# Optimization experiments

Hardware: AMD Instinct MI355X
Metric: run time of the kernel (lower is better)

Reference implementation:

```python
import jax, jax.numpy as jnp
import numpy as np

N = 100000
E = 1600000
IN_C, HID_C, OUT_C = 64, 128, 64


def sage_conv(x, edge_index, W_l, b_l, W_r):
    # PyG SAGEConv (mean aggr): out = lin_l(mean_{j in N(i)} x_j) + lin_r(x_i)
    src, dst = edge_index[0], edge_index[1]
    n = x.shape[0]
    msg = x[src]                                        # [E, C] gather
    agg = jax.ops.segment_sum(msg, dst, num_segments=n) # [N, C] scatter-add
    deg = jax.ops.segment_sum(jnp.ones((msg.shape[0],), x.dtype), dst, num_segments=n)
    agg = agg / jnp.maximum(deg, 1.0)[:, None]          # mean, deg-0 safe
    return agg @ W_l.T + b_l + x @ W_r.T


def setup_inputs() -> dict:
    key = jax.random.key(0)
    ks = jax.random.split(key, 8)
    x = jax.random.normal(ks[0], (N, IN_C), dtype=jnp.float32)
    edge_index = jax.random.randint(ks[1], (2, E), 0, N)
    s1 = 1.0 / np.sqrt(IN_C)
    s2 = 1.0 / np.sqrt(HID_C)
    W1_l = jax.random.uniform(ks[2], (HID_C, IN_C), jnp.float32, -s1, s1)
    W1_r = jax.random.uniform(ks[3], (HID_C, IN_C), jnp.float32, -s1, s1)
    b1 = jax.random.uniform(ks[4], (HID_C,), jnp.float32, -s1, s1)
    W2_l = jax.random.uniform(ks[5], (OUT_C, HID_C), jnp.float32, -s2, s2)
    W2_r = jax.random.uniform(ks[6], (OUT_C, HID_C), jnp.float32, -s2, s2)
    b2 = jax.random.uniform(ks[7], (OUT_C,), jnp.float32, -s2, s2)
    return {"x": x, "edge_index": edge_index, "W1_l": W1_l, "W1_r": W1_r,
            "b1": b1, "W2_l": W2_l, "W2_r": W2_r, "b2": b2}


def reference(x, edge_index, W1_l, W1_r, b1, W2_l, W2_r, b2):
    h = sage_conv(x, edge_index, W1_l, b1, W1_r)
    h = jax.nn.relu(h)
    h = sage_conv(h, edge_index, W2_l, b2, W2_r)
    return jax.nn.sigmoid(h)
```

## Files before the change

kernel.cpp:

```cpp
#include <hip/hip_runtime.h>
#include <math.h>

#define IN_C 64
#define HID_C 128
#define OUT_C 64
#define NBK 256
#define BD 64
#define GS 16

typedef __attribute__((ext_vector_type(8))) short bf16x8;
typedef __attribute__((ext_vector_type(4))) float f32x4;

__device__ __forceinline__ unsigned short f2bf(float f) {
  unsigned u = __float_as_uint(f);
  u = (u + 0x7FFFu + ((u >> 16) & 1u)) >> 16;
  return (unsigned short)u;
}
__device__ __forceinline__ float bf2f(unsigned v) {
  return __uint_as_float(v << 16);
}
__device__ __forceinline__ unsigned pack2(float a, float b) {
  return (unsigned)f2bf(a) | ((unsigned)f2bf(b) << 16);
}

__global__ __launch_bounds__(256) void k_xb(const int* __restrict__ dst,
                                            int* __restrict__ bh,
                                            const float4* __restrict__ x4,
                                            uint2* __restrict__ xh2,
                                            int E, int Mreal, int Mtot) {
  __shared__ int hh[NBK];
  int t = threadIdx.x;
  if (blockIdx.x < 1024) {
    hh[t] = 0;
    __syncthreads();
    for (int e = blockIdx.x * 256 + t; e < E; e += 1024 * 256)
      atomicAdd(&hh[dst[e] >> 9], 1);
    __syncthreads();
    if (hh[t]) atomicAdd(&bh[t * GS], hh[t]);
  } else {
    int b = blockIdx.x - 1024;
    for (int i = b * 256 + t; i < Mtot; i += 2048 * 256) {
      uint2 p = {0u, 0u};
      if (i < Mreal) {
        float4 v = x4[i];
        p.x = pack2(v.x, v.y);
        p.y = pack2(v.z, v.w);
      }
      xh2[i] = p;
    }
  }
}

__global__ __launch_bounds__(256) void k_bscan(const int* __restrict__ bh,
                                               int* __restrict__ bstart,
                                               int* __restrict__ rstart,
                                               int* __restrict__ gcur) {
  __shared__ int s1[NBK], s2[NBK];
  int t = threadIdx.x;
  int cnt = bh[t * GS];
  int region = 16 * min(cnt, (cnt >> 4) + 512);
  int creg = cnt + 4096;
  s1[t] = region; s2[t] = creg;
  __syncthreads();
  for (int off = 1; off < NBK; off <<= 1) {
    int a1 = (t >= off) ? s1[t - off] : 0;
    int a2 = (t >= off) ? s2[t - off] : 0;
    __syncthreads();
    s1[t] += a1; s2[t] += a2;
    __syncthreads();
  }
  int ex1 = s1[t] - region;
  int ex2 = s2[t] - creg;
  bstart[t] = ex1; gcur[t * GS] = ex1; rstart[t] = ex2;
}

__global__ __launch_bounds__(256) void k_msplit(const int* __restrict__ src,
                                                const int* __restrict__ dst,
                                                int* __restrict__ gcur,
                                                int* __restrict__ ebuf, int E) {
  __shared__ int bcnt[NBK], bhead[NBK];
  __shared__ int bins[BD][NBK];
  int t = threadIdx.x;
  bcnt[t] = 0; bhead[t] = 0;
  int per = (E + gridDim.x - 1) / gridDim.x;
  int e0 = blockIdx.x * per, e1 = min(E, e0 + per);
  int e = e0 + t;
  int pb[8], pv[8]; int pc = 0;
  __syncthreads();
  for (;;) {
    while (pc < 8 && e < e1) {
      int d = dst[e], s = src[e];
      pb[pc] = d >> 9; pv[pc] = (s << 9) | (d & 511);
      pc++; e += 256;
    }
    for (int q = pc - 1; q >= 0; --q) {
      int pos = atomicAdd(&bcnt[pb[q]], 1);
      if (pos < BD) {
        bins[(bhead[pb[q]] + pos) & (BD - 1)][pb[q]] = pv[q];
        pc--;
        if (q != pc) { pb[q] = pb[pc]; pv[q] = pv[pc]; }
      }
    }
    int pending = __syncthreads_count(pc > 0 || e < e1);
    int cntv = min(bcnt[t], BD);
    int head = bhead[t];
    while (cntv >= 16) {
      int base = atomicAdd(&gcur[t * GS], 16);
      int4 o[4];
#pragma unroll
      for (int k = 0; k < 16; ++k)
        ((int*)o)[k] = bins[(head + k) & (BD - 1)][t];
      int4* g = (int4*)(ebuf + base);
      g[0] = o[0]; g[1] = o[1]; g[2] = o[2]; g[3] = o[3];
      head = (head + 16) & (BD - 1);
      cntv -= 16;
    }
    bhead[t] = head;
    bcnt[t] = cntv;
    __syncthreads();
    if (!pending) break;
  }
  int cntv = bcnt[t];
  if (cntv > 0) {
    int head = bhead[t];
    int base = atomicAdd(&gcur[t * GS], 16);
#pragma unroll
    for (int k = 0; k < 16; ++k)
      ebuf[base + k] = (k < cntv) ? bins[(head + k) & (BD - 1)][t] : -1;
  }
}

__global__ __launch_bounds__(512) void k_localcsr(const int* __restrict__ ebuf,
                                                  const int* __restrict__ bstart,
                                                  const int* __restrict__ gcur,
                                                  const int* __restrict__ rstart,
                                                  int* __restrict__ csr,
                                                  int* __restrict__ row_start,
                                                  int* __restrict__ rend,
                                                  float* __restrict__ invd, int N) {
  __shared__ int lcnt[512], loff[512], lcur[512];
  int t = threadIdx.x, b = blockIdx.x;
  int start = bstart[b], endp = gcur[b * GS], rs = rstart[b];
  lcnt[t] = 0;
  __syncthreads();
  for (int i = start + t; i < endp; i += 512) {
    int pe = ebuf[i];
    if (pe != -1) atomicAdd(&lcnt[pe & 511], 1);
  }
  __syncthreads();
  int v = lcnt[t];
  int pvn = (v + 7) & ~7;
  loff[t] = pvn;
  __syncthreads();
  for (int off = 1; off < 512; off <<= 1) {
    int a = (t >= off) ? loff[t - off] : 0;
    __syncthreads();
    loff[t] += a;
    __syncthreads();
  }
  int ex = loff[t] - pvn;
  lcur[t] = ex;
  int node = (b << 9) + t;
  if (node < N) {
    row_start[node] = rs + ex;
    rend[node] = rs + ex + pvn;
    invd[node] = 1.0f / fmaxf((float)v, 1.0f);
  }
  __syncthreads();
  for (int i = start + t; i < endp; i += 512) {
    int pe = ebuf[i];
    if (pe != -1) {
      int pos = atomicAdd(&lcur[pe & 511], 1);
      csr[rs + pos] = pe >> 9;
    }
  }
  for (int k = ex + v; k < ex + pvn; ++k) csr[rs + k] = N;
}

__global__ __launch_bounds__(256) void k_gather1(const uint4* __restrict__ xh4,
                                                 const int* __restrict__ csr,
                                                 const int* __restrict__ row_start,
                                                 const int* __restrict__ rend,
                                                 const float* __restrict__ invd,
                                                 uint4* __restrict__ aggh4, int N) {
  int node = (blockIdx.x * 256 + threadIdx.x) >> 3;
  if (node >= N) return;
  int c = threadIdx.x & 7;
  int lb = threadIdx.x & 56;
  int j = row_start[node], end = rend[node];
  float a0 = 0, a1 = 0, a2 = 0, a3 = 0, a4 = 0, a5 = 0, a6 = 0, a7 = 0;
  for (; j < end; j += 8) {
    int sv = csr[j + c];
#pragma unroll
    for (int k = 0; k < 8; ++k) {
      int s = __shfl(sv, lb + k);
      uint4 v = xh4[s * 8 + c];
      a0 += bf2f(v.x & 0xffffu); a1 += bf2f(v.x >> 16);
      a2 += bf2f(v.y & 0xffffu); a3 += bf2f(v.y >> 16);
      a4 += bf2f(v.z & 0xffffu); a5 += bf2f(v.z >> 16);
      a6 += bf2f(v.w & 0xffffu); a7 += bf2f(v.w >> 16);
    }
  }
  float inv = invd[node];
  uint4 p;
  p.x = pack2(a0 * inv, a1 * inv);
  p.y = pack2(a2 * inv, a3 * inv);
  p.z = pack2(a4 * inv, a5 * inv);
  p.w = pack2(a6 * inv, a7 * inv);
  aggh4[node * 8 + c] = p;
}

__global__ __launch_bounds__(512, 1) void k_lin12(
    const unsigned short* __restrict__ aggh, const unsigned short* __restrict__ xh,
    const float* __restrict__ W1l, const float* __restrict__ W1r,
    const float* __restrict__ b1, const float* __restrict__ W2l,
    const float* __restrict__ W2r, const float* __restrict__ b2,
    unsigned short* __restrict__ zh, float* __restrict__ r, int N) {
  __shared__ __align__(16) unsigned short sW1[128 * 136];
  __shared__ __align__(16) unsigned short sW2[128 * 136];
  __shared__ __align__(16) unsigned short sAH[128 * 136];
  __shared__ float sb[128];
  __shared__ float sb2[64];
  int t = threadIdx.x;
  if (blockIdx.x == 0 && t < 32) ((unsigned*)zh)[N * 32 + t] = 0;
  for (int i = t; i < 128 * 128; i += 512) {
    int o = i >> 7, k = i & 127;
    float w1 = (k < 64) ? W1l[o * 64 + k] : W1r[o * 64 + (k - 64)];
    sW1[o * 136 + k] = f2bf(w1);
    float w2 = (o < 64) ? W2l[o * 128 + k] : W2r[(o - 64) * 128 + k];
    sW2[o * 136 + k] = f2bf(w2);
  }
  if (t < 128) sb[t] = b1[t];
  else if (t < 192) sb2[t - 128] = b2[t - 128];
  int lane = t & 63, qm = lane >> 4, ln = lane & 15;
  int m0 = (t >> 6) * 16;
  __syncthreads();

  int ntiles = (N + 127) >> 7;
  for (int tile = blockIdx.x; tile < ntiles; tile += gridDim.x) {
    int base = tile << 7;
    for (int i = t; i < 128 * 64; i += 512) {
      int n = i >> 6, uu = i & 63;
      int node = base + n;
      unsigned v = 0;
      if (node < N) v = (uu < 32) ? ((const unsigned*)aggh)[node * 32 + uu]
                                  : ((const unsigned*)xh)[node * 32 + (uu - 32)];
      ((unsigned*)(sAH + n * 136))[uu] = v;
    }
    __syncthreads();
    bf16x8 af[4];
#pragma unroll
    for (int kc = 0; kc < 4; ++kc)
      af[kc] = *(const bf16x8*)(sAH + (m0 + ln) * 136 + kc * 32 + qm * 8);
#pragma unroll
    for (int ot = 0; ot < 8; ++ot) {
      int o0 = ot * 16;
      f32x4 acc = {0.f, 0.f, 0.f, 0.f};
#pragma unroll
      for (int kc = 0; kc < 4; ++kc) {
        bf16x8 wfr = *(const bf16x8*)(sW1 + (o0 + ln) * 136 + kc * 32 + qm * 8);
        acc = __builtin_amdgcn_mfma_f32_16x16x32_bf16(wfr, af[kc], acc, 0, 0, 0);
      }
      int ob = o0 + qm * 4;
      float h0 = fmaxf(acc[0] + sb[ob + 0], 0.f);
      float h1 = fmaxf(acc[1] + sb[ob + 1], 0.f);
      float h2 = fmaxf(acc[2] + sb[ob + 2], 0.f);
      float h3 = fmaxf(acc[3] + sb[ob + 3], 0.f);
      unsigned* hd = (unsigned*)(sAH + (m0 + ln) * 136 + ob);
      hd[0] = pack2(h0, h1);
      hd[1] = pack2(h2, h3);
    }
    bf16x8 af2[4];
#pragma unroll
    for (int kc = 0; kc < 4; ++kc)
      af2[kc] = *(const bf16x8*)(sAH + (m0 + ln) * 136 + kc * 32 + qm * 8);
#pragma unroll
    for (int ot = 0; ot < 8; ++ot) {
      int o0 = ot * 16;
      f32x4 acc = {0.f, 0.f, 0.f, 0.f};
#pragma unroll
      for (int kc = 0; kc < 4; ++kc) {
        bf16x8 wfr = *(const bf16x8*)(sW2 + (o0 + ln) * 136 + kc * 32 + qm * 8);
        acc = __builtin_amdgcn_mfma_f32_16x16x32_bf16(wfr, af2[kc], acc, 0, 0, 0);
      }
      int node = base + m0 + ln;
      int u = o0 + qm * 4;
      if (node < N) {
        if (u < 64) {
          uint2 zv;
          zv.x = pack2(acc[0], acc[1]);
          zv.y = pack2(acc[2], acc[3]);
          *(uint2*)(zh + node * 64 + u) = zv;
        } else {
          int ub = u - 64;
          float4 rv;
          rv.x = acc[0] + sb2[ub + 0];
          rv.y = acc[1] + sb2[ub + 1];
          rv.z = acc[2] + sb2[ub + 2];
          rv.w = acc[3] + sb2[ub + 3];
          *(float4*)(r + node * 64 + ub) = rv;
        }
      }
    }
    __syncthreads();
  }
}

__global__ __launch_bounds__(256) void k_gather2b(const uint4* __restrict__ zh4,
                                                  const float* __restrict__ r,
                                                  const int* __restrict__ csr,
                                                  const int* __restrict__ row_start,
                                                  const int* __restrict__ rend,
                                                  const float* __restrict__ invd,
                                                  float* __restrict__ out, int N) {
  int node = (blockIdx.x * 256 + threadIdx.x) >> 3;
  if (node >= N) return;
  int c = threadIdx.x & 7;
  int lb = threadIdx.x & 56;
  int j = row_start[node], end = rend[node];
  float a0 = 0, a1 = 0, a2 = 0, a3 = 0, a4 = 0, a5 = 0, a6 = 0, a7 = 0;
  for (; j < end; j += 8) {
    int sv = csr[j + c];
#pragma unroll
    for (int k = 0; k < 8; ++k) {
      int s = __shfl(sv, lb + k);
      uint4 v = zh4[s * 8 + c];
      a0 += bf2f(v.x & 0xffffu); a1 += bf2f(v.x >> 16);
      a2 += bf2f(v.y & 0xffffu); a3 += bf2f(v.y >> 16);
      a4 += bf2f(v.z & 0xffffu); a5 += bf2f(v.z >> 16);
      a6 += bf2f(v.w & 0xffffu); a7 += bf2f(v.w >> 16);
    }
  }
  float inv = invd[node];
  const float4* r4 = (const float4*)r;
  float4* o4 = (float4*)out;
  int bi = node * 16 + c * 2;
  float4 r0 = r4[bi], r1 = r4[bi + 1];
  float4 w0, w1;
  w0.x = 1.0f / (1.0f + __expf(-(a0 * inv + r0.x)));
  w0.y = 1.0f / (1.0f + __expf(-(a1 * inv + r0.y)));
  w0.z = 1.0f / (1.0f + __expf(-(a2 * inv + r0.z)));
  w0.w = 1.0f / (1.0f + __expf(-(a3 * inv + r0.w)));
  w1.x = 1.0f / (1.0f + __expf(-(a4 * inv + r1.x)));
  w1.y = 1.0f / (1.0f + __expf(-(a5 * inv + r1.y)));
  w1.z = 1.0f / (1.0f + __expf(-(a6 * inv + r1.z)));
  w1.w = 1.0f / (1.0f + __expf(-(a7 * inv + r1.w)));
  o4[bi] = w0;
  o4[bi + 1] = w1;
}

extern "C" void kernel_launch(void* const* d_in, const int* in_sizes, int n_in,
                              void* d_out, int out_size, void* d_ws, size_t ws_size,
                              hipStream_t stream) {
  const float* x   = (const float*)d_in[0];
  const int*   ei  = (const int*)d_in[1];
  const float* W1l = (const float*)d_in[2];
  const float* W1r = (const float*)d_in[3];
  const float* b1  = (const float*)d_in[4];
  const float* W2l = (const float*)d_in[5];
  const float* W2r = (const float*)d_in[6];
  const float* b2  = (const float*)d_in[7];
  float* out = (float*)d_out;

  int N = in_sizes[0] / IN_C;
  int E = in_sizes[1] / 2;
  const int* src = ei;
  const int* dst = ei + E;

  char* ws = (char*)d_ws;
  size_t off = 0;
  auto alignup = [](size_t v) { return (v + 511) & ~(size_t)511; };
  int* bh = (int*)(ws + off);         off = alignup(off + NBK * GS * 4);
  int* gcur = (int*)(ws + off);       off = alignup(off + NBK * GS * 4);
  int* bstart = (int*)(ws + off);     off = alignup(off + NBK * 4);
  int* rstart = (int*)(ws + off);     off = alignup(off + NBK * 4);
  int* csr = (int*)(ws + off);        off = alignup(off + ((size_t)E + NBK * 4096) * 4);
  int* row_start = (int*)(ws + off);  off = alignup(off + (size_t)N * 4);
  int* rend = (int*)(ws + off);       off = alignup(off + (size_t)N * 4);
  float* invd = (float*)(ws + off);   off = alignup(off + (size_t)N * 4);
  unsigned short* xh = (unsigned short*)(ws + off);   off = alignup(off + (size_t)(N + 1) * 64 * 2);
  unsigned short* aggh = (unsigned short*)(ws + off); off = alignup(off + (size_t)N * 64 * 2);
  unsigned short* zh = (unsigned short*)(ws + off);   off = alignup(off + (size_t)(N + 1) * 64 * 2);
  float* rbuf = (float*)(ws + off);   off = alignup(off + (size_t)N * 64 * 4);
  int* ebuf = (int*)aggh;

  hipMemsetAsync(bh, 0, NBK * GS * 4, stream);
  k_xb<<<3072, 256, 0, stream>>>(dst, bh, (const float4*)x, (uint2*)xh,
                                 E, N * 16, (N + 1) * 16);
  k_bscan<<<1, NBK, 0, stream>>>(bh, bstart, rstart, gcur);
  k_msplit<<<512, 256, 0, stream>>>(src, dst, gcur, ebuf, E);
  k_localcsr<<<NBK, 512, 0, stream>>>(ebuf, bstart, gcur, rstart, csr,
                                      row_start, rend, invd, N);

  k_gather1<<<(N + 31) / 32, 256, 0, stream>>>((const uint4*)xh, csr, row_start,
                                               rend, invd, (uint4*)aggh, N);
  k_lin12<<<256, 512, 0, stream>>>(aggh, xh, W1l, W1r, b1, W2l, W2r, b2,
                                   zh, rbuf, N);
  k_gather2b<<<(N + 31) / 32, 256, 0, stream>>>((const uint4*)zh, rbuf, csr,
                                                row_start, rend, invd, out, N);
}
```

Measured before the change: 271.4 us.

## Keep weight fragments in registers and swizzle LDS tiles in fused linear kernel

The fused two-layer linear kernel now holds the W1 and W2 MFMA fragments in registers, one 16-output slice per wave, instead of staging both weight matrices in shared memory. Each wave iterates over the node rows of the tile rather than over output tiles. Tiles are loaded with 16-byte vector loads into XOR-swizzled LDS buffers to avoid bank conflicts, and biases are kept in registers. Less LDS per block, a raised occupancy hint and a doubled grid are meant to allow more resident blocks, at the cost of extra register pressure and an added barrier between the two layers.

```diff
diff --git a/kernel.cpp b/kernel.cpp
--- a/kernel.cpp
+++ b/kernel.cpp
@@ -210,81 +210,78 @@
   aggh4[node * 8 + c] = p;
 }
 
-__global__ __launch_bounds__(512, 1) void k_lin12(
-    const unsigned short* __restrict__ aggh, const unsigned short* __restrict__ xh,
+__global__ __launch_bounds__(512, 4) void k_lin12(
+    const uint4* __restrict__ aggh4, const uint4* __restrict__ xh4,
     const float* __restrict__ W1l, const float* __restrict__ W1r,
     const float* __restrict__ b1, const float* __restrict__ W2l,
     const float* __restrict__ W2r, const float* __restrict__ b2,
     unsigned short* __restrict__ zh, float* __restrict__ r, int N) {
-  __shared__ __align__(16) unsigned short sW1[128 * 136];
-  __shared__ __align__(16) unsigned short sW2[128 * 136];
-  __shared__ __align__(16) unsigned short sAH[128 * 136];
-  __shared__ float sb[128];
-  __shared__ float sb2[64];
+  __shared__ __align__(16) char sA[128 * 256];
+  __shared__ __align__(16) char sH[128 * 256];
   int t = threadIdx.x;
   if (blockIdx.x == 0 && t < 32) ((unsigned*)zh)[N * 32 + t] = 0;
-  for (int i = t; i < 128 * 128; i += 512) {
-    int o = i >> 7, k = i & 127;
-    float w1 = (k < 64) ? W1l[o * 64 + k] : W1r[o * 64 + (k - 64)];
-    sW1[o * 136 + k] = f2bf(w1);
-    float w2 = (o < 64) ? W2l[o * 128 + k] : W2r[(o - 64) * 128 + k];
-    sW2[o * 136 + k] = f2bf(w2);
-  }
-  if (t < 128) sb[t] = b1[t];
-  else if (t < 192) sb2[t - 128] = b2[t - 128];
-  int lane = t & 63, qm = lane >> 4, ln = lane & 15;
-  int m0 = (t >> 6) * 16;
-  __syncthreads();
+  int w = t >> 6, lane = t & 63, qm = lane >> 4, ln = lane & 15;
+  bf16x8 w1f[4], w2f[4];
+  int o = w * 16 + ln;
+#pragma unroll
+  for (int kc = 0; kc < 4; ++kc) {
+    int k0 = kc * 32 + qm * 8;
+    bf16x8 v1, v2;
+#pragma unroll
+    for (int j = 0; j < 8; ++j) {
+      int kk = k0 + j;
+      float f1 = (kk < 64) ? W1l[o * 64 + kk] : W1r[o * 64 + (kk - 64)];
+      float f2 = (o < 64) ? W2l[o * 128 + kk] : W2r[(o - 64) * 128 + kk];
+      v1[j] = (short)f2bf(f1);
+      v2[j] = (short)f2bf(f2);
+    }
+    w1f[kc] = v1; w2f[kc] = v2;
+  }
+  float4 b1v = *(const float4*)(b1 + w * 16 + qm * 4);
+  int u = w * 16 + qm * 4;
+  float4 b2v = {0.f, 0.f, 0.f, 0.f};
+  if (u >= 64) b2v = *(const float4*)(b2 + (u - 64));
 
   int ntiles = (N + 127) >> 7;
   for (int tile = blockIdx.x; tile < ntiles; tile += gridDim.x) {
     int base = tile << 7;
-    for (int i = t; i < 128 * 64; i += 512) {
-      int n = i >> 6, uu = i & 63;
-      int node = base + n;
-      unsigned v = 0;
-      if (node < N) v = (uu < 32) ? ((const unsigned*)aggh)[node * 32 + uu]
-                                  : ((const unsigned*)xh)[node * 32 + (uu - 32)];
-      ((unsigned*)(sAH + n * 136))[uu] = v;
-    }
-    __syncthreads();
-    bf16x8 af[4];
-#pragma unroll
-    for (int kc = 0; kc < 4; ++kc)
-      af[kc] = *(const bf16x8*)(sAH + (m0 + ln) * 136 + kc * 32 + qm * 8);
-#pragma unroll
-    for (int ot = 0; ot < 8; ++ot) {
-      int o0 = ot * 16;
+#pragma unroll
+    for (int rep = 0; rep < 4; ++rep) {
+      int i = rep * 512 + t;
+      int row = i >> 4, ch = i & 15;
+      int node = base + row;
+      uint4 v = {0u, 0u, 0u, 0u};
+      if (node < N) v = (ch < 8) ? aggh4[node * 8 + ch] : xh4[node * 8 + (ch - 8)];
+      *(uint4*)(sA + row * 256 + ((ch * 16) ^ ((row & 7) << 4))) = v;
+    }
+    __syncthreads();
+#pragma unroll
+    for (int g = 0; g < 8; ++g) {
+      int row = g * 16 + ln;
+      int rb = row * 256, sw = (row & 7) << 4;
       f32x4 acc = {0.f, 0.f, 0.f, 0.f};
 #pragma unroll
       for (int kc = 0; kc < 4; ++kc) {
-        bf16x8 wfr = *(const bf16x8*)(sW1 + (o0 + ln) * 136 + kc * 32 + qm * 8);
-        acc = __builtin_amdgcn_mfma_f32_16x16x32_bf16(wfr, af[kc], acc, 0, 0, 0);
-      }
-      int ob = o0 + qm * 4;
-      float h0 = fmaxf(acc[0] + sb[ob + 0], 0.f);
-      float h1 = fmaxf(acc[1] + sb[ob + 1], 0.f);
-      float h2 = fmaxf(acc[2] + sb[ob + 2], 0.f);
-      float h3 = fmaxf(acc[3] + sb[ob + 3], 0.f);
-      unsigned* hd = (unsigned*)(sAH + (m0 + ln) * 136 + ob);
-      hd[0] = pack2(h0, h1);
-      hd[1] = pack2(h2, h3);
-    }
-    bf16x8 af2[4];
-#pragma unroll
-    for (int kc = 0; kc < 4; ++kc)
-      af2[kc] = *(const bf16x8*)(sAH + (m0 + ln) * 136 + kc * 32 + qm * 8);
-#pragma unroll
-    for (int ot = 0; ot < 8; ++ot) {
-      int o0 = ot * 16;
+        bf16x8 af = *(const bf16x8*)(sA + rb + ((kc * 64 + qm * 16) ^ sw));
+        acc = __builtin_amdgcn_mfma_f32_16x16x32_bf16(w1f[kc], af, acc, 0, 0, 0);
+      }
+      uint2 hp;
+      hp.x = pack2(fmaxf(acc[0] + b1v.x, 0.f), fmaxf(acc[1] + b1v.y, 0.f));
+      hp.y = pack2(fmaxf(acc[2] + b1v.z, 0.f), fmaxf(acc[3] + b1v.w, 0.f));
+      *(uint2*)(sH + rb + ((w * 32 + qm * 8) ^ sw)) = hp;
+    }
+    __syncthreads();
+#pragma unroll
+    for (int g = 0; g < 8; ++g) {
+      int row = g * 16 + ln;
+      int rb = row * 256, sw = (row & 7) << 4;
       f32x4 acc = {0.f, 0.f, 0.f, 0.f};
 #pragma unroll
       for (int kc = 0; kc < 4; ++kc) {
-        bf16x8 wfr = *(const bf16x8*)(sW2 + (o0 + ln) * 136 + kc * 32 + qm * 8);
-        acc = __builtin_amdgcn_mfma_f32_16x16x32_bf16(wfr, af2[kc], acc, 0, 0, 0);
-      }
-      int node = base + m0 + ln;
-      int u = o0 + qm * 4;
+        bf16x8 hf = *(const bf16x8*)(sH + rb + ((kc * 64 + qm * 16) ^ sw));
+        acc = __builtin_amdgcn_mfma_f32_16x16x32_bf16(w2f[kc], hf, acc, 0, 0, 0);
+      }
+      int node = base + row;
       if (node < N) {
         if (u < 64) {
           uint2 zv;
@@ -292,13 +289,10 @@
           zv.y = pack2(acc[2], acc[3]);
           *(uint2*)(zh + node * 64 + u) = zv;
         } else {
-          int ub = u - 64;
           float4 rv;
-          rv.x = acc[0] + sb2[ub + 0];
-          rv.y = acc[1] + sb2[ub + 1];
-          rv.z = acc[2] + sb2[ub + 2];
-          rv.w = acc[3] + sb2[ub + 3];
-          *(float4*)(r + node * 64 + ub) = rv;
+          rv.x = acc[0] + b2v.x; rv.y = acc[1] + b2v.y;
+          rv.z = acc[2] + b2v.z; rv.w = acc[3] + b2v.w;
+          *(float4*)(r + node * 64 + (u - 64)) = rv;
         }
       }
     }
@@ -394,8 +388,8 @@
 
   k_gather1<<<(N + 31) / 32, 256, 0, stream>>>((const uint4*)xh, csr, row_start,
                                                rend, invd, (uint4*)aggh, N);
-  k_lin12<<<256, 512, 0, stream>>>(aggh, xh, W1l, W1r, b1, W2l, W2r, b2,
-                                   zh, rbuf, N);
+  k_lin12<<<512, 512, 0, stream>>>((const uint4*)aggh, (const uint4*)xh,
+                                   W1l, W1r, b1, W2l, W2r, b2, zh, rbuf, N);
   k_gather2b<<<(N + 31) / 32, 256, 0, stream>>>((const uint4*)zh, rbuf, csr,
                                                 row_start, rend, invd, out, N);
 }
```

Result: slower. 277.1 us (+2.1%).
